# Kernel optimization log

Hardware: AMD Instinct MI355X
Metric: run time of the kernel (lower is better)

Reference implementation:

```python
import jax, jax.numpy as jnp
import numpy as np

SR = 48000.0


def _lin_interp(x, n):
    # Matches torch F.interpolate(mode='linear', align_corners=False) on last axis.
    T = x.shape[-1]
    pos = (jnp.arange(n, dtype=jnp.float32) + 0.5) * (T / n) - 0.5
    pos = jnp.clip(pos, 0.0, T - 1)
    i0 = jnp.floor(pos).astype(jnp.int32)
    i1 = jnp.minimum(i0 + 1, T - 1)
    w = (pos - i0.astype(jnp.float32)).astype(x.dtype)
    return jnp.take(x, i0, axis=-1) * (1.0 - w) + jnp.take(x, i1, axis=-1) * w


def setup_inputs() -> dict:
    key = jax.random.key(0)
    k1, k2, k3 = jax.random.split(key, 3)
    B, T, N = 16, 250, 100
    harm_amps = jax.random.uniform(k1, (B, T, N), dtype=jnp.float32)
    # realistic fundamental frequencies: 80..480 Hz
    f0_hz = 80.0 + 400.0 * jax.random.uniform(k2, (B, T), dtype=jnp.float32)
    # small inharmonicity coefficients (piano-like): ~0..1e-4
    inh = 1e-4 * jax.random.uniform(k3, (B,), dtype=jnp.float32)
    return {"harm_amps": harm_amps, "f0_hz": f0_hz, "inh": inh, "n_samples": 48000}


def reference(harm_amps, f0_hz, inh, n_samples):
    B, T, N = harm_amps.shape
    # upsample amplitudes (B,N,n_samples) and f0 (B,n_samples)
    a = _lin_interp(jnp.transpose(harm_amps, (0, 2, 1)), n_samples)
    f0_up = _lin_interp(f0_hz, n_samples)
    k = jnp.arange(1, N + 1, dtype=jnp.float32)  # harmonic numbers 1..N
    stretch = jnp.sqrt(1.0 + inh[:, None] * k ** 2)  # (B,N)
    inst_freq = f0_up[:, None, :] * (k[None, :] * stretch)[:, :, None]  # (B,N,n)
    nyq_mask = (inst_freq < SR * 0.45).astype(a.dtype)
    phase = jnp.cumsum(2.0 * jnp.pi * inst_freq / SR, axis=-1)
    signal = jnp.sum(a * nyq_mask * jnp.sin(phase), axis=1, keepdims=True)  # (B,1,n)
    return signal / N
```

## Files before the change

kernel.cpp:

```cpp
#include <hip/hip_runtime.h>
#include <cmath>

#pragma clang fp contract(off)

#define SRF   48000.0f
#define NYQF  21600.0f
constexpr float  TWO_PI_F  = 6.283185307179586476925286766559f;
constexpr double INV_2PI_D = 0.15915494309189533576888376337251;
constexpr float  RC1 = (float)INV_2PI_D;
constexpr float  RC2 = (float)(INV_2PI_D - (double)RC1);
constexpr double INV_SR_D = 1.0 / 48000.0;
constexpr float  DD1 = (float)INV_SR_D;
constexpr float  DD2 = (float)(INV_SR_D - (double)DD1);

__device__ __forceinline__ float hsin_rev(float r) {
#if __has_builtin(__builtin_amdgcn_sinf)
    return __builtin_amdgcn_sinf(r);
#else
    return __sinf(r * TWO_PI_F);
#endif
}

__device__ __forceinline__ float div48000(float t) {
    float h = t * DD1;
    float r = __builtin_fmaf(t, DD1, -h);
    float s = __builtin_fmaf(t, DD2, r);
    return h + s;
}

__device__ __forceinline__ float sin_phase(float ph) {
    float h  = ph * RC1;
    float r  = __builtin_fmaf(ph, RC1, -h);
    float s  = __builtin_fmaf(ph, RC2, r);
    float nn = __builtin_rintf(h);
    float fr = (h - nn) + s;
    return hsin_rev(fr);
}

template <int IDX>
__device__ __forceinline__ float grp4_bcast(float v, int lb) {
#if __has_builtin(__builtin_amdgcn_ds_swizzle)
    constexpr int imm = (IDX << 5) | 0x1C;
    return __int_as_float(__builtin_amdgcn_ds_swizzle(__float_as_int(v), imm));
#else
    return __shfl(v, lb + IDX);
#endif
}

__device__ __forceinline__ float kcval(int k, float ib) {
    float kf = (float)(k + 1);
    float k2 = kf * kf;
    float m  = ib * k2;
    float s1 = 1.0f + m;
    float st = (float)sqrt((double)s1);
    return kf * st;
}

__global__ void __launch_bounds__(256) k_f0up(const float* __restrict__ f0,
        float* __restrict__ f0up, float* __restrict__ out,
        int T, int n, float pf) {
    int j = blockIdx.x * 256 + threadIdx.x;
    int b = blockIdx.y;
    if (j >= n) return;
    float pos = ((float)j + 0.5f);
    pos = pos * pf;
    pos = pos - 0.5f;
    pos = fmaxf(pos, 0.0f);
    pos = fminf(pos, (float)(T - 1));
    int   i0 = (int)pos;
    int   i1 = min(i0 + 1, T - 1);
    float w  = pos - (float)i0;
    float omw = 1.0f - w;
    const float* fb = f0 + b * T;
    f0up[(size_t)b * n + j] = fb[i0] * omw + fb[i1] * w;
    out[(size_t)b * n + j]  = 0.0f;
}

__global__ void __launch_bounds__(256) k_scan4(const float* __restrict__ f0up,
        const float* __restrict__ inh, float* __restrict__ scan4,
        int N, int n) {
    __shared__ float lv[6016];
    const int k   = blockIdx.x;
    const int b   = blockIdx.y;
    const int tid = threadIdx.x;
    const float kc = kcval(k, inh[b]);
    const float4* f4 = (const float4*)(f0up + (size_t)b * n);
    const int len4 = n >> 4;

    auto l2of = [&](float4 v) -> float {
        float a0 = div48000(TWO_PI_F * (kc * v.x));
        float a1 = div48000(TWO_PI_F * (kc * v.y));
        float a2 = div48000(TWO_PI_F * (kc * v.z));
        float a3 = div48000(TWO_PI_F * (kc * v.w));
        return (a0 + a1) + (a2 + a3);
    };
    for (int i = tid; i < len4; i += 256) {
        float s01 = l2of(f4[4*i])     + l2of(f4[4*i + 1]);
        float s23 = l2of(f4[4*i + 2]) + l2of(f4[4*i + 3]);
        lv[i] = s01 + s23;
    }
    __syncthreads();

    int offp = 0, lenp = len4, P = 4;
    for (int l = 5; ; ++l) {
        int lenc = lenp >> 1;
        int offc = offp + lenp;
        for (int i = tid; i < lenc; i += 256)
            lv[offc + i] = lv[offp + 2*i] + lv[offp + 2*i + 1];
        __syncthreads();
        P = l;
        if (lenc == 1) break;
        offp = offc; lenp = lenc;
    }
    for (int l = P - 1; l >= 4; --l) {
        int lenl = n >> l;
        int offl = 0;
        for (int m = 4; m < l; ++m) offl += (n >> m);
        int offh = offl + lenl;
        int lenh = n >> (l + 1);
        float*       arr = lv + offl;
        const float* hi  = lv + offh;
        for (int i = tid; i < lenh; i += 256) {
            float v = hi[i];
            int e = 2*i + 2;
            if (e < lenl) arr[e] = v + arr[e];
            arr[2*i + 1] = v;
        }
        __syncthreads();
    }
    float* sp = scan4 + (size_t)(b * N + k) * (len4 + 1);
    if (tid == 0) sp[0] = 0.0f;
    for (int i = tid; i < len4; i += 256) sp[1 + i] = lv[i];
}

__global__ void __launch_bounds__(256) k_synth4(
        const float* __restrict__ harm, const float* __restrict__ f0up,
        const float* __restrict__ inh,  const float* __restrict__ scan4,
        float* __restrict__ out, int B, int T, int N, int n, float pf, int kpg) {
    const int tid  = threadIdx.x;
    const int b    = blockIdx.y;
    const int k0   = blockIdx.z * kpg;
    const int g    = blockIdx.x * 256 + tid;
    const int q    = g >> 2;
    const int c    = g & 3;
    const int NG   = n >> 4;
    const int NGP  = NG + 1;
    const int kend = min(k0 + kpg, N);
    const int kact = kend - k0;
    const bool valid = q < NG;

    __shared__ float2 amps[8 * 32];
    __shared__ float  kcs[32];
    __shared__ float  xp[4][256];

    const float ib    = inh[b];
    const float tmaxf = (float)(T - 1);
    for (int i = tid; i < kact; i += 256) kcs[i] = kcval(k0 + i, ib);

    const int j0blk = blockIdx.x * 1024;
    int i0min;
    {
        float p = ((float)j0blk + 0.5f);
        p = p * pf; p = p - 0.5f;
        p = fmaxf(p, 0.0f); p = fminf(p, tmaxf);
        i0min = (int)p;
    }
    for (int idx = tid; idx < 8 * kact; idx += 256) {
        int r = idx / kact, kk = idx - r * kact;
        int r0 = min(i0min + r, T - 1);
        int r1 = min(i0min + r + 1, T - 1);
        float a0 = harm[((size_t)b * T + r0) * N + (k0 + kk)];
        float a1 = harm[((size_t)b * T + r1) * N + (k0 + kk)];
        amps[idx] = make_float2(a0, a1 - a0);
    }
    __syncthreads();

    float u0=0.f,u1=0.f,u2=0.f,u3=0.f;
    float w0=0.f,w1=0.f,w2=0.f,w3=0.f;
    int   a0o=0,a1o=0,a2o=0,a3o=0;
    float acc0=0.f, acc1=0.f, acc2=0.f, acc3=0.f;
    float um = __builtin_inff();
    if (valid) {
        const float4 v = *(const float4*)(f0up + (size_t)b * n + (size_t)q * 16 + c * 4);
        u0=v.x; u1=v.y; u2=v.z; u3=v.w;
        um = fminf(fminf(u0,u1), fminf(u2,u3));
        const int jb = q * 16 + c * 4;
        #pragma unroll
        for (int i = 0; i < 4; ++i) {
            float p = ((float)(jb + i) + 0.5f);
            p = p * pf; p = p - 0.5f;
            p = fmaxf(p, 0.0f); p = fminf(p, tmaxf);
            int i0 = (int)p;
            float wv = p - (float)i0;
            int aoo  = (i0 - i0min) * kact;
            if (i==0){w0=wv;a0o=aoo;}
            else if (i==1){w1=wv;a1o=aoo;}
            else if (i==2){w2=wv;a2o=aoo;}
            else {w3=wv;a3o=aoo;}
        }
    }
    #pragma unroll
    for (int off = 32; off > 0; off >>= 1)
        um = fminf(um, __shfl_xor(um, off));
    const float umin = um;
    const int lb = (tid & 63) & ~3;

    if (valid) {
        const float* s4k = scan4 + (size_t)(b * N + k0) * NGP;
        float g0c = s4k[q];
        float g1c = s4k[q + 1];

        for (int k = k0; k < kend; ++k) {
            const int   kk = k - k0;
            const float kc = kcs[kk];
            if (kc * umin >= NYQF) break;
            const float G0 = g0c, G1 = g1c;
            if (k + 1 < kend) {
                const float* nx = s4k + NGP;
                g0c = nx[q];
                g1c = nx[q + 1];
                s4k = nx;
            }

            float x0 = div48000(TWO_PI_F * (kc * u0));
            float x1 = div48000(TWO_PI_F * (kc * u1));
            float x2 = div48000(TWO_PI_F * (kc * u2));
            float x3 = div48000(TWO_PI_F * (kc * u3));
            float L1p = x0 + x1, L1q = x2 + x3;
            float L2  = L1p + L1q;

            float s0 = grp4_bcast<0>(L2, lb);
            float s1 = grp4_bcast<1>(L2, lb);
            float s2 = grp4_bcast<2>(L2, lb);
            float t01 = s0 + s1;
            float b1v = G0 + s0;
            float b2v = G0 + t01;
            float b3v = b2v + s2;
            float base = (c == 0) ? G0  : (c == 1) ? b1v : (c == 2) ? b2v : b3v;
            float bn   = (c == 0) ? b1v : (c == 1) ? b2v : (c == 2) ? b3v : G1;

            float ph0 = base + x0;
            float ph1 = base + L1p;
            float ph2 = ph1 + x2;
            float ph3 = bn;

            {   float t1 = kc * u0;
                if (t1 < NYQF) { float sv = sin_phase(ph0);
                    float2 a = amps[a0o + kk];
                    acc0 = __builtin_fmaf(__builtin_fmaf(w0, a.y, a.x), sv, acc0); } }
            {   float t1 = kc * u1;
                if (t1 < NYQF) { float sv = sin_phase(ph1);
                    float2 a = amps[a1o + kk];
                    acc1 = __builtin_fmaf(__builtin_fmaf(w1, a.y, a.x), sv, acc1); } }
            {   float t1 = kc * u2;
                if (t1 < NYQF) { float sv = sin_phase(ph2);
                    float2 a = amps[a2o + kk];
                    acc2 = __builtin_fmaf(__builtin_fmaf(w2, a.y, a.x), sv, acc2); } }
            {   float t1 = kc * u3;
                if (t1 < NYQF) { float sv = sin_phase(ph3);
                    float2 a = amps[a3o + kk];
                    acc3 = __builtin_fmaf(__builtin_fmaf(w3, a.y, a.x), sv, acc3); } }
        }
    }

    {
        const int wid  = tid >> 6;
        const int lane = tid & 63;
        *(float4*)&xp[wid][4 * lane] = make_float4(acc0, acc1, acc2, acc3);
        const float Nf = (float)N;
        const int jb = blockIdx.x * 1024 + wid * 256;
        float* ob = out + (size_t)b * n + jb;
        #pragma unroll
        for (int i = 0; i < 4; ++i) {
            float v  = xp[wid][i * 64 + lane];
            int   jj = jb + i * 64 + lane;
            if (jj < n) atomicAdd(&ob[i * 64 + lane], v / Nf);
        }
    }
}

__global__ void __launch_bounds__(256) k_scan_synth(
        const float* __restrict__ harm, const float* __restrict__ f0up,
        const float* __restrict__ inh,  float* __restrict__ out,
        int B, int T, int N, int n, float pf) {
    extern __shared__ float lv[];
    const int k   = blockIdx.x;
    const int b   = blockIdx.y;
    const int tid = threadIdx.x;
    const float kc = kcval(k, inh[b]);
    const float* fb = f0up + (size_t)b * n;

    auto inc = [&](int j) -> float {
        float u    = fb[j];
        float inst = kc * u;
        float tt   = TWO_PI_F * inst;
        return tt / SRF;
    };

    const int len1 = n >> 1;
    {
        const float4* f4 = (const float4*)fb;
        for (int i = tid; i < (n >> 2); i += 256) {
            float4 u = f4[i];
            float a0 = (TWO_PI_F * (kc * u.x)) / SRF;
            float a1 = (TWO_PI_F * (kc * u.y)) / SRF;
            float a2 = (TWO_PI_F * (kc * u.z)) / SRF;
            float a3 = (TWO_PI_F * (kc * u.w)) / SRF;
            lv[i] = (a0 + a1) + (a2 + a3);
        }
    }
    __syncthreads();
    int offp = 0, lenp = n >> 2, P = 2;
    for (int l = 3; ; ++l) {
        int lenc = lenp >> 1;
        int offc = offp + lenp;
        for (int i = tid; i < lenc; i += 256)
            lv[offc + i] = lv[offp + 2*i] + lv[offp + 2*i + 1];
        __syncthreads();
        P = l;
        if (lenc == 1) break;
        offp = offc; lenp = lenc;
    }
    for (int l = P - 1; l >= 2; --l) {
        int lenl = n >> l;
        int offl = 0;
        for (int m = 2; m < l; ++m) offl += (n >> m);
        float*       arr = lv + offl;
        const float* hi  = lv + offl + lenl;
        int lenh = n >> (l + 1);
        for (int i = tid; i < lenh; i += 256) {
            float v = hi[i];
            int e = 2*i + 2;
            if (e < lenl) arr[e] = v + arr[e];
            arr[2*i + 1] = v;
        }
        __syncthreads();
    }
    const float* scan2 = lv;

    const float  tmaxf = (float)(T - 1);
    const float  invN  = 1.0f / (float)N;
    const float* hb    = harm + (size_t)b * T * N + k;
    float*       ob    = out + (size_t)b * n;

    auto emit = [&](int j, float ph) {
        float u    = fb[j];
        float inst = kc * u;
        if (!(inst < NYQF)) return;
        double pr = (double)ph * INV_2PI_D;
        double fr = pr - rint(pr);
        float  sv = hsin_rev((float)fr);
        float pos = ((float)j + 0.5f);
        pos = pos * pf; pos = pos - 0.5f;
        pos = fmaxf(pos, 0.0f); pos = fminf(pos, tmaxf);
        int   i0 = (int)pos;
        int   i1 = min(i0 + 1, T - 1);
        float w  = pos - (float)i0;
        float a  = hb[(size_t)i0 * N] * (1.0f - w) + hb[(size_t)i1 * N] * w;
        atomicAdd(&ob[j], (a * sv) * invN);
    };

    if (tid == 0) emit(0, inc(0));
    for (int tt = tid; tt < len1; tt += 256) {
        float s1;
        if (tt == 0)      s1 = inc(0) + inc(1);
        else if (tt & 1)  s1 = scan2[(tt - 1) >> 1];
        else              s1 = scan2[(tt >> 1) - 1] + (inc(2*tt) + inc(2*tt + 1));
        emit(2*tt + 1, s1);
        int je = 2*tt + 2;
        if (je < n) emit(je, s1 + inc(je));
    }
}

extern "C" void kernel_launch(void* const* d_in, const int* in_sizes, int n_in,
                              void* d_out, int out_size, void* d_ws, size_t ws_size,
                              hipStream_t stream) {
    const int B = in_sizes[2];
    const int T = in_sizes[1] / B;
    const int N = in_sizes[0] / (B * T);
    const int n = out_size / B;
    const float pf = (float)((double)T / (double)n);

    const float* harm = (const float*)d_in[0];
    const float* f0   = (const float*)d_in[1];
    const float* inh  = (const float*)d_in[2];
    float* out  = (float*)d_out;
    float* f0up = (float*)d_ws;

    const int KZ  = 4;
    const int kpg = (N + KZ - 1) / KZ;
    const int NG  = n / 16;
    const size_t needFast = (size_t)B * n * 4 + (size_t)B * N * (NG + 1) * 4;
    const bool fast = (ws_size >= needFast) && (n % 16 == 0) && (kpg <= 32);

    k_f0up<<<dim3((n + 255) / 256, B), 256, 0, stream>>>(f0, f0up, out, T, n, pf);

    if (fast) {
        float* scan4 = (float*)((char*)d_ws + (size_t)B * n * 4);
        k_scan4<<<dim3(N, B), 256, 0, stream>>>(f0up, inh, scan4, N, n);
        const int tiles = (NG * 4 + 255) / 256;
        k_synth4<<<dim3(tiles, B, KZ), 256, 0, stream>>>(
            harm, f0up, inh, scan4, out, B, T, N, n, pf, kpg);
    } else {
        const size_t lds_bytes = (size_t)(n / 2) * sizeof(float);
        k_scan_synth<<<dim3(N, B), 256, lds_bytes, stream>>>(
            harm, f0up, inh, out, B, T, N, n, pf);
    }
}
```

Baseline: 137.8 us.

## Fuse f0 upsampling into scan and synth kernels, shrink scan sync tail

Removes the separate f0 upsampling kernel on the fast path. The scan and synth kernels now interpolate f0 directly from the low-rate input instead of reading an upsampled buffer, and output zeroing moves into the scan kernel, split across the k blocks. The small upper levels of the up-sweep and down-sweep tree run inside a single wavefront without block barriers. This saves one launch and a global round trip through f0up, at the cost of recomputing the interpolation, which does gathers from a small array, in every block.

```diff
diff --git a/kernel.cpp b/kernel.cpp
--- a/kernel.cpp
+++ b/kernel.cpp
@@ -56,70 +56,111 @@
     return kf * st;
 }
 
+__device__ __forceinline__ float f0interp(const float* __restrict__ fb,
+        int j, int T, float pf, float tmaxf) {
+    float pos = ((float)j + 0.5f);
+    pos = pos * pf;
+    pos = pos - 0.5f;
+    pos = fmaxf(pos, 0.0f);
+    pos = fminf(pos, tmaxf);
+    int   i0 = (int)pos;
+    int   i1 = min(i0 + 1, T - 1);
+    float w  = pos - (float)i0;
+    float omw = 1.0f - w;
+    return fb[i0] * omw + fb[i1] * w;
+}
+
 __global__ void __launch_bounds__(256) k_f0up(const float* __restrict__ f0,
         float* __restrict__ f0up, float* __restrict__ out,
         int T, int n, float pf) {
     int j = blockIdx.x * 256 + threadIdx.x;
     int b = blockIdx.y;
     if (j >= n) return;
-    float pos = ((float)j + 0.5f);
-    pos = pos * pf;
-    pos = pos - 0.5f;
-    pos = fmaxf(pos, 0.0f);
-    pos = fminf(pos, (float)(T - 1));
-    int   i0 = (int)pos;
-    int   i1 = min(i0 + 1, T - 1);
-    float w  = pos - (float)i0;
-    float omw = 1.0f - w;
     const float* fb = f0 + b * T;
-    f0up[(size_t)b * n + j] = fb[i0] * omw + fb[i1] * w;
+    f0up[(size_t)b * n + j] = f0interp(fb, j, T, pf, (float)(T - 1));
     out[(size_t)b * n + j]  = 0.0f;
 }
 
-__global__ void __launch_bounds__(256) k_scan4(const float* __restrict__ f0up,
+__global__ void __launch_bounds__(256) k_scan4(const float* __restrict__ f0,
         const float* __restrict__ inh, float* __restrict__ scan4,
-        int N, int n) {
+        float* __restrict__ outz, int N, int n, int T, float pf) {
     __shared__ float lv[6016];
     const int k   = blockIdx.x;
     const int b   = blockIdx.y;
     const int tid = threadIdx.x;
     const float kc = kcval(k, inh[b]);
-    const float4* f4 = (const float4*)(f0up + (size_t)b * n);
+    const float* fb = f0 + b * T;
+    const float tmaxf = (float)(T - 1);
     const int len4 = n >> 4;
 
-    auto l2of = [&](float4 v) -> float {
-        float a0 = div48000(TWO_PI_F * (kc * v.x));
-        float a1 = div48000(TWO_PI_F * (kc * v.y));
-        float a2 = div48000(TWO_PI_F * (kc * v.z));
-        float a3 = div48000(TWO_PI_F * (kc * v.w));
+    {
+        const int chunk = (n + N - 1) / N;
+        const int z0 = k * chunk;
+        for (int i = tid; i < chunk; i += 256) {
+            int j = z0 + i;
+            if (j < n) outz[(size_t)b * n + j] = 0.0f;
+        }
+    }
+
+    auto l2of = [&](int jb) -> float {
+        float a0 = div48000(TWO_PI_F * (kc * f0interp(fb, jb + 0, T, pf, tmaxf)));
+        float a1 = div48000(TWO_PI_F * (kc * f0interp(fb, jb + 1, T, pf, tmaxf)));
+        float a2 = div48000(TWO_PI_F * (kc * f0interp(fb, jb + 2, T, pf, tmaxf)));
+        float a3 = div48000(TWO_PI_F * (kc * f0interp(fb, jb + 3, T, pf, tmaxf)));
         return (a0 + a1) + (a2 + a3);
     };
     for (int i = tid; i < len4; i += 256) {
-        float s01 = l2of(f4[4*i])     + l2of(f4[4*i + 1]);
-        float s23 = l2of(f4[4*i + 2]) + l2of(f4[4*i + 3]);
+        float s01 = l2of(16 * i)     + l2of(16 * i + 4);
+        float s23 = l2of(16 * i + 8) + l2of(16 * i + 12);
         lv[i] = s01 + s23;
     }
     __syncthreads();
 
-    int offp = 0, lenp = len4, P = 4;
-    for (int l = 5; ; ++l) {
-        int lenc = lenp >> 1;
-        int offc = offp + lenp;
+    int P = 4; { int L = len4; while (L > 1) { L >>= 1; ++P; } }
+
+    int offp = 0, lenp = len4;
+    while ((lenp >> 1) > 64) {
+        int lenc = lenp >> 1, offc = offp + lenp;
         for (int i = tid; i < lenc; i += 256)
             lv[offc + i] = lv[offp + 2*i] + lv[offp + 2*i + 1];
         __syncthreads();
-        P = l;
-        if (lenc == 1) break;
         offp = offc; lenp = lenc;
     }
+
+    if (tid < 64) {
+        int op = offp, lp = lenp;
+        while (lp > 1) {
+            int lc = lp >> 1, oc = op + lp;
+            for (int i = tid; i < lc; i += 64)
+                lv[oc + i] = lv[op + 2*i] + lv[op + 2*i + 1];
+            op = oc; lp = lc;
+        }
+        for (int l = P - 1; l >= 4; --l) {
+            int lenh = n >> (l + 1);
+            if (lenh > 64) break;
+            int lenl = n >> l;
+            int offl = 0;
+            for (int m = 4; m < l; ++m) offl += (n >> m);
+            float*       arr = lv + offl;
+            const float* hi  = lv + offl + lenl;
+            for (int i = tid; i < lenh; i += 64) {
+                float v = hi[i];
+                int e = 2*i + 2;
+                if (e < lenl) arr[e] = v + arr[e];
+                arr[2*i + 1] = v;
+            }
+        }
+    }
+    __syncthreads();
+
     for (int l = P - 1; l >= 4; --l) {
+        int lenh = n >> (l + 1);
+        if (lenh <= 64) continue;
         int lenl = n >> l;
         int offl = 0;
         for (int m = 4; m < l; ++m) offl += (n >> m);
-        int offh = offl + lenl;
-        int lenh = n >> (l + 1);
         float*       arr = lv + offl;
-        const float* hi  = lv + offh;
+        const float* hi  = lv + offl + lenl;
         for (int i = tid; i < lenh; i += 256) {
             float v = hi[i];
             int e = 2*i + 2;
@@ -128,13 +169,14 @@
         }
         __syncthreads();
     }
+
     float* sp = scan4 + (size_t)(b * N + k) * (len4 + 1);
     if (tid == 0) sp[0] = 0.0f;
     for (int i = tid; i < len4; i += 256) sp[1 + i] = lv[i];
 }
 
 __global__ void __launch_bounds__(256) k_synth4(
-        const float* __restrict__ harm, const float* __restrict__ f0up,
+        const float* __restrict__ harm, const float* __restrict__ f0,
         const float* __restrict__ inh,  const float* __restrict__ scan4,
         float* __restrict__ out, int B, int T, int N, int n, float pf, int kpg) {
     const int tid  = threadIdx.x;
@@ -181,9 +223,7 @@
     float acc0=0.f, acc1=0.f, acc2=0.f, acc3=0.f;
     float um = __builtin_inff();
     if (valid) {
-        const float4 v = *(const float4*)(f0up + (size_t)b * n + (size_t)q * 16 + c * 4);
-        u0=v.x; u1=v.y; u2=v.z; u3=v.w;
-        um = fminf(fminf(u0,u1), fminf(u2,u3));
+        const float* fb = f0 + b * T;
         const int jb = q * 16 + c * 4;
         #pragma unroll
         for (int i = 0; i < 4; ++i) {
@@ -191,13 +231,17 @@
             p = p * pf; p = p - 0.5f;
             p = fmaxf(p, 0.0f); p = fminf(p, tmaxf);
             int i0 = (int)p;
+            int i1 = min(i0 + 1, T - 1);
             float wv = p - (float)i0;
+            float omw = 1.0f - wv;
+            float uv = fb[i0] * omw + fb[i1] * wv;
             int aoo  = (i0 - i0min) * kact;
-            if (i==0){w0=wv;a0o=aoo;}
-            else if (i==1){w1=wv;a1o=aoo;}
-            else if (i==2){w2=wv;a2o=aoo;}
-            else {w3=wv;a3o=aoo;}
-        }
+            if (i==0){u0=uv;w0=wv;a0o=aoo;}
+            else if (i==1){u1=uv;w1=wv;a1o=aoo;}
+            else if (i==2){u2=uv;w2=wv;a2o=aoo;}
+            else {u3=uv;w3=wv;a3o=aoo;}
+        }
+        um = fminf(fminf(u0,u1), fminf(u2,u3));
     }
     #pragma unroll
     for (int off = 32; off > 0; off >>= 1)
@@ -393,15 +437,14 @@
     const size_t needFast = (size_t)B * n * 4 + (size_t)B * N * (NG + 1) * 4;
     const bool fast = (ws_size >= needFast) && (n % 16 == 0) && (kpg <= 32);
 
-    k_f0up<<<dim3((n + 255) / 256, B), 256, 0, stream>>>(f0, f0up, out, T, n, pf);
-
     if (fast) {
         float* scan4 = (float*)((char*)d_ws + (size_t)B * n * 4);
-        k_scan4<<<dim3(N, B), 256, 0, stream>>>(f0up, inh, scan4, N, n);
+        k_scan4<<<dim3(N, B), 256, 0, stream>>>(f0, inh, scan4, out, N, n, T, pf);
         const int tiles = (NG * 4 + 255) / 256;
         k_synth4<<<dim3(tiles, B, KZ), 256, 0, stream>>>(
-            harm, f0up, inh, scan4, out, B, T, N, n, pf, kpg);
+            harm, f0, inh, scan4, out, B, T, N, n, pf, kpg);
     } else {
+        k_f0up<<<dim3((n + 255) / 256, B), 256, 0, stream>>>(f0, f0up, out, T, n, pf);
         const size_t lds_bytes = (size_t)(n / 2) * sizeof(float);
         k_scan_synth<<<dim3(N, B), 256, lds_bytes, stream>>>(
             harm, f0up, inh, out, B, T, N, n, pf);
```

Result: slower. 167.9 us (+21.8%).

## Store prefix scan at 32-sample granularity and reconstruct odd groups via swizzle

Applied to the files above, without the earlier changes.

The scan kernel now writes prefix sums every 32 samples instead of every 16, which halves the scan4 workspace written and read. In the synth kernel each thread loads one prefix value per harmonic instead of two. Odd 16-sample groups rebuild their base from the neighbouring even group's value plus its local sum, using an 8-lane swizzle broadcast. This trades global memory traffic for a few extra adds and one cross-lane op per harmonic. It also tightens the fast-path condition to n divisible by 32.

```diff
diff --git a/kernel.cpp b/kernel.cpp
--- a/kernel.cpp
+++ b/kernel.cpp
@@ -44,6 +44,14 @@
     return __int_as_float(__builtin_amdgcn_ds_swizzle(__float_as_int(v), imm));
 #else
     return __shfl(v, lb + IDX);
+#endif
+}
+
+__device__ __forceinline__ float grp8_bcast0(float v, int lane) {
+#if __has_builtin(__builtin_amdgcn_ds_swizzle)
+    return __int_as_float(__builtin_amdgcn_ds_swizzle(__float_as_int(v), 0x0018));
+#else
+    return __shfl(v, lane & ~7);
 #endif
 }
 
@@ -86,6 +94,7 @@
     const float kc = kcval(k, inh[b]);
     const float4* f4 = (const float4*)(f0up + (size_t)b * n);
     const int len4 = n >> 4;
+    const int len5 = n >> 5;
 
     auto l2of = [&](float4 v) -> float {
         float a0 = div48000(TWO_PI_F * (kc * v.x));
@@ -112,7 +121,7 @@
         if (lenc == 1) break;
         offp = offc; lenp = lenc;
     }
-    for (int l = P - 1; l >= 4; --l) {
+    for (int l = P - 1; l >= 5; --l) {
         int lenl = n >> l;
         int offl = 0;
         for (int m = 4; m < l; ++m) offl += (n >> m);
@@ -128,9 +137,10 @@
         }
         __syncthreads();
     }
-    float* sp = scan4 + (size_t)(b * N + k) * (len4 + 1);
+    float* sp = scan4 + (size_t)(b * N + k) * (len5 + 1);
     if (tid == 0) sp[0] = 0.0f;
-    for (int i = tid; i < len4; i += 256) sp[1 + i] = lv[i];
+    const float* s5 = lv + len4;
+    for (int i = tid; i < len5; i += 256) sp[1 + i] = s5[i];
 }
 
 __global__ void __launch_bounds__(256) k_synth4(
@@ -144,10 +154,12 @@
     const int q    = g >> 2;
     const int c    = g & 3;
     const int NG   = n >> 4;
-    const int NGP  = NG + 1;
+    const int NG5P = (n >> 5) + 1;
     const int kend = min(k0 + kpg, N);
     const int kact = kend - k0;
     const bool valid = q < NG;
+    const bool oddq  = (q & 1) != 0;
+    const int  si    = (q >> 1) + (q & 1);
 
     __shared__ float2 amps[8 * 32];
     __shared__ float  kcs[32];
@@ -203,22 +215,21 @@
     for (int off = 32; off > 0; off >>= 1)
         um = fminf(um, __shfl_xor(um, off));
     const float umin = um;
-    const int lb = (tid & 63) & ~3;
+    const int lane = tid & 63;
+    const int lb   = lane & ~3;
 
     if (valid) {
-        const float* s4k = scan4 + (size_t)(b * N + k0) * NGP;
-        float g0c = s4k[q];
-        float g1c = s4k[q + 1];
+        const float* s4k = scan4 + (size_t)(b * N + k0) * NG5P;
+        float svc = s4k[si];
 
         for (int k = k0; k < kend; ++k) {
             const int   kk = k - k0;
             const float kc = kcs[kk];
             if (kc * umin >= NYQF) break;
-            const float G0 = g0c, G1 = g1c;
+            const float Sv = svc;
             if (k + 1 < kend) {
-                const float* nx = s4k + NGP;
-                g0c = nx[q];
-                g1c = nx[q + 1];
+                const float* nx = s4k + NG5P;
+                svc = nx[si];
                 s4k = nx;
             }
 
@@ -232,7 +243,15 @@
             float s0 = grp4_bcast<0>(L2, lb);
             float s1 = grp4_bcast<1>(L2, lb);
             float s2 = grp4_bcast<2>(L2, lb);
+            float s3 = grp4_bcast<3>(L2, lb);
             float t01 = s0 + s1;
+            float s23 = s2 + s3;
+            float L4v = t01 + s23;
+            float G1e = Sv + L4v;
+            float Gx  = grp8_bcast0(G1e, lane);
+            float G0  = oddq ? Gx : Sv;
+            float G1  = oddq ? Sv : G1e;
+
             float b1v = G0 + s0;
             float b2v = G0 + t01;
             float b3v = b2v + s2;
@@ -265,7 +284,6 @@
 
     {
         const int wid  = tid >> 6;
-        const int lane = tid & 63;
         *(float4*)&xp[wid][4 * lane] = make_float4(acc0, acc1, acc2, acc3);
         const float Nf = (float)N;
         const int jb = blockIdx.x * 1024 + wid * 256;
@@ -390,8 +408,9 @@
     const int KZ  = 4;
     const int kpg = (N + KZ - 1) / KZ;
     const int NG  = n / 16;
-    const size_t needFast = (size_t)B * n * 4 + (size_t)B * N * (NG + 1) * 4;
-    const bool fast = (ws_size >= needFast) && (n % 16 == 0) && (kpg <= 32);
+    const int NG5 = n / 32;
+    const size_t needFast = (size_t)B * n * 4 + (size_t)B * N * (NG5 + 1) * 4;
+    const bool fast = (ws_size >= needFast) && (n % 32 == 0) && (kpg <= 32);
 
     k_f0up<<<dim3((n + 255) / 256, B), 256, 0, stream>>>(f0, f0up, out, T, n, pf);
 
```

After: 136.7 us. About the same (-0.8%).
